# Kernel tuning notes

Hardware: AMD Instinct MI355X
Metric: run time of the kernel (lower is better)

The kernel has to match this reference:

```python
import jax, jax.numpy as jnp
import numpy as np

B = 1_000_000
S = 5          # no_sensors
I = S + 3      # linear in_features


def setup_inputs() -> dict:
    key = jax.random.key(0)
    k = jax.random.split(key, 9)
    x = jax.random.uniform(k[0], (B, S), dtype=jnp.float32)
    W1d = jax.random.normal(k[1], (B, 3, I), dtype=jnp.float32) * 0.5
    W1m = jax.random.normal(k[2], (B, 3, I), dtype=jnp.float32) * 0.5
    s1d = jax.random.uniform(k[3], (B, 3), dtype=jnp.float32)   # previous layer1d_output
    s1m = jax.random.uniform(k[4], (B, 3), dtype=jnp.float32)   # previous layer1m_output
    excitatory_rule = jnp.where(jax.random.bernoulli(k[5], 0.5, (3, I)), 1.0, -1.0).astype(jnp.float32)
    learning_rate = jnp.full((3, I), 0.05, dtype=jnp.float32)
    driving_rule = jax.random.randint(k[6], (3, I), 0, 2, dtype=jnp.int32)
    learning_rule = jax.random.randint(k[7], (3, I), 0, 4, dtype=jnp.int32)
    return {"x": x, "W1d": W1d, "W1m": W1m, "s1d": s1d, "s1m": s1m,
            "excitatory_rule": excitatory_rule, "learning_rate": learning_rate,
            "driving_rule": driving_rule, "learning_rule": learning_rule}


def reference(x, W1d, W1m, s1d, s1m, excitatory_rule, learning_rate, driving_rule, learning_rule):
    # forward (batched over B agents)
    x1 = jnp.concatenate([x, s1d], axis=1)                       # [B, I]
    x2 = jnp.concatenate([x, s1m], axis=1)                       # [B, I]
    out1 = jax.nn.sigmoid(jnp.einsum('bij,bj->bi', W1d, x1))     # driving activation
    out2 = 0.5 * jax.nn.sigmoid(jnp.einsum('bij,bj->bi', W1m, x2)) + 0.5  # modulatory

    lr = learning_rate[None]      # [1,3,I]
    rule = learning_rule[None]    # [1,3,I]
    exc = excitatory_rule[None]   # [1,3,I]

    def updated(W, xv, yv):
        # per-element Hebbian-family update, vectorized over [B,3,I]
        xb = xv[:, None, :]   # x[j] broadcast over output unit i
        yb = yv[:, :, None]   # y[i] broadcast over input j
        w = jnp.abs(W)        # torch code first assigns abs(w), then uses it in the rule
        hebb = lr * xb * yb * (1 - w)
        post = lr * (w * (xb - 1) * yb + (1 - w) * xb * yb)
        pre  = lr * (w * xb * (yb - 1) + (1 - w) * xb * yb)
        d = jnp.tanh(4 * (1 - jnp.abs(xb - yb) - 2))
        cov = lr * jnp.where(d > 0, d * (1 - w), d * w)
        delta = jnp.select([rule == 0, rule == 1, rule == 2], [hebb, post, pre], cov)
        wn = w + delta
        # sign-flip if excitatory_rule * w < 0
        return jnp.where(exc * wn < 0, wn * exc, wn)

    drive = (driving_rule == 1)[None]                            # [1,3,I]
    W1d_new = jnp.where(drive, updated(W1d, x1, out1), W1d)
    W1m_new = jnp.where(drive, W1m, updated(W1m, x2, out2))

    output = (out1 * out1)[:, 1:]                                # squared, drop unit 0 -> [B,2]
    return output, W1d_new, W1m_new, out1, out2
```

## Files before the change

kernel.cpp:

```cpp
#include <hip/hip_runtime.h>
#include <math.h>


__device__ __forceinline__ float upd_elem(float W, float xb, float yb,
                                          float lr, int rule, float exc) {
    float w = fabsf(W);
    float delta;
    if (rule == 0) {
        delta = lr * xb * yb * (1.f - w);
    } else if (rule == 1) {
        delta = lr * (w * (xb - 1.f) * yb + (1.f - w) * xb * yb);
    } else if (rule == 2) {
        delta = lr * (w * xb * (yb - 1.f) + (1.f - w) * xb * yb);
    } else {
        float d = tanhf(4.f * (1.f - fabsf(xb - yb) - 2.f));
        delta = lr * ((d > 0.f) ? d * (1.f - w) : d * w);
    }
    float wn = w + delta;
    return (exc * wn < 0.f) ? wn * exc : wn;
}

__global__ __launch_bounds__(256) void nn_plastic_kernel(
    const float* __restrict__ x,
    const float* __restrict__ W1d,
    const float* __restrict__ W1m,
    const float* __restrict__ s1d,
    const float* __restrict__ s1m,
    const float* __restrict__ exc_t,
    const float* __restrict__ lr_t,
    const int*   __restrict__ drive_t,
    const int*   __restrict__ rule_t,
    float* __restrict__ out,
    int B)
{
    int b = blockIdx.x * blockDim.x + threadIdx.x;
    if (b >= B) return;

    float x1[8], x2[8];
#pragma unroll
    for (int j = 0; j < 5; ++j) {
        float v = x[b * 5 + j];
        x1[j] = v; x2[j] = v;
    }
#pragma unroll
    for (int j = 0; j < 3; ++j) {
        x1[5 + j] = s1d[b * 3 + j];
        x2[5 + j] = s1m[b * 3 + j];
    }

    float4 wd[6], wm[6];
    const float4* W1d4 = reinterpret_cast<const float4*>(W1d) + (size_t)b * 6;
    const float4* W1m4 = reinterpret_cast<const float4*>(W1m) + (size_t)b * 6;
#pragma unroll
    for (int k = 0; k < 6; ++k) { wd[k] = W1d4[k]; wm[k] = W1m4[k]; }
    float* wdf = reinterpret_cast<float*>(wd);
    float* wmf = reinterpret_cast<float*>(wm);

    float out1[3], out2[3];
#pragma unroll
    for (int i = 0; i < 3; ++i) {
        float a1 = 0.f, a2 = 0.f;
#pragma unroll
        for (int j = 0; j < 8; ++j) {
            a1 = fmaf(wdf[i * 8 + j], x1[j], a1);
            a2 = fmaf(wmf[i * 8 + j], x2[j], a2);
        }
        out1[i] = 1.f / (1.f + expf(-a1));
        out2[i] = 0.5f / (1.f + expf(-a2)) + 0.5f;
    }

#pragma unroll
    for (int i = 0; i < 3; ++i) {
#pragma unroll
        for (int j = 0; j < 8; ++j) {
            const int k = i * 8 + j;
            const float lr  = lr_t[k];
            const float exc = exc_t[k];
            const int   rul = rule_t[k];
            const int   drv = drive_t[k];
            if (drv == 1) {
                wdf[k] = upd_elem(wdf[k], x1[j], out1[i], lr, rul, exc);
            } else {
                wmf[k] = upd_elem(wmf[k], x2[j], out2[i], lr, rul, exc);
            }
        }
    }

    float* out_o  = out;
    float* out_wd = out + (size_t)B * 2;
    float* out_wm = out + (size_t)B * 26;
    float* out_o1 = out + (size_t)B * 50;
    float* out_o2 = out + (size_t)B * 53;

    float4* wd_out4 = reinterpret_cast<float4*>(out_wd) + (size_t)b * 6;
    float4* wm_out4 = reinterpret_cast<float4*>(out_wm) + (size_t)b * 6;
#pragma unroll
    for (int k = 0; k < 6; ++k) { wd_out4[k] = wd[k]; wm_out4[k] = wm[k]; }

    float2 o = make_float2(out1[1] * out1[1], out1[2] * out1[2]);
    reinterpret_cast<float2*>(out_o)[b] = o;
#pragma unroll
    for (int i = 0; i < 3; ++i) {
        out_o1[b * 3 + i] = out1[i];
        out_o2[b * 3 + i] = out2[i];
    }
}

extern "C" void kernel_launch(void* const* d_in, const int* in_sizes, int n_in,
                              void* d_out, int out_size, void* d_ws, size_t ws_size,
                              hipStream_t stream) {
    const float* x    = (const float*)d_in[0];
    const float* W1d  = (const float*)d_in[1];
    const float* W1m  = (const float*)d_in[2];
    const float* s1d  = (const float*)d_in[3];
    const float* s1m  = (const float*)d_in[4];
    const float* exc  = (const float*)d_in[5];
    const float* lr   = (const float*)d_in[6];
    const int*   drv  = (const int*)d_in[7];
    const int*   rul  = (const int*)d_in[8];
    float* out = (float*)d_out;

    const int B = in_sizes[0] / 5;
    const int block = 256;
    const int grid = (B + block - 1) / block;
    nn_plastic_kernel<<<grid, block, 0, stream>>>(
        x, W1d, W1m, s1d, s1m, exc, lr, drv, rul, out, B);
}
```

Baseline: 410.9 us.

## Stage weight matrices through LDS with coalesced direct-to-LDS loads and stores

Each block now loads its slice of W1d and W1m into shared memory with global_load_lds in a fully coalesced pattern, and each thread reads its 24 weights from LDS. Updated weights go back to LDS and are written out coalesced after a barrier. This replaces the strided per-thread float4 accesses, which spanned 96 bytes per thread. It costs 48KB of LDS per block, adds two barriers, and the launch-bounds hint of 3 waves may limit occupancy.

Result: faster. 400.4 us (-2.6%).

```diff
diff --git a/kernel.cpp b/kernel.cpp
--- a/kernel.cpp
+++ b/kernel.cpp
@@ -1,6 +1,13 @@
 #include <hip/hip_runtime.h>
 #include <math.h>
 
+
+__device__ __forceinline__ void gload_lds16(const float* g, float* lds) {
+    __builtin_amdgcn_global_load_lds(
+        (const __attribute__((address_space(1))) void*)g,
+        (__attribute__((address_space(3))) void*)lds,
+        16, 0, 0);
+}
 
 __device__ __forceinline__ float upd_elem(float W, float xb, float yb,
                                           float lr, int rule, float exc) {
@@ -20,7 +27,7 @@
     return (exc * wn < 0.f) ? wn * exc : wn;
 }
 
-__global__ __launch_bounds__(256) void nn_plastic_kernel(
+__global__ __launch_bounds__(256, 3) void nn_plastic_kernel(
     const float* __restrict__ x,
     const float* __restrict__ W1d,
     const float* __restrict__ W1m,
@@ -33,76 +40,117 @@
     float* __restrict__ out,
     int B)
 {
-    int b = blockIdx.x * blockDim.x + threadIdx.x;
-    if (b >= B) return;
+    __shared__ float wA[6144];
+    __shared__ float wB[6144];
 
-    float x1[8], x2[8];
+    const int t = threadIdx.x;
+    const long long b      = (long long)blockIdx.x * 256 + t;
+    const long long total4 = (long long)B * 6;
+    const long long base4  = (long long)blockIdx.x * 1536;
+    const bool act = (b < (long long)B);
+
+    const float4* W1d4 = (const float4*)W1d;
+    const float4* W1m4 = (const float4*)W1m;
 #pragma unroll
-    for (int j = 0; j < 5; ++j) {
-        float v = x[b * 5 + j];
-        x1[j] = v; x2[j] = v;
-    }
-#pragma unroll
-    for (int j = 0; j < 3; ++j) {
-        x1[5 + j] = s1d[b * 3 + j];
-        x2[5 + j] = s1m[b * 3 + j];
-    }
-
-    float4 wd[6], wm[6];
-    const float4* W1d4 = reinterpret_cast<const float4*>(W1d) + (size_t)b * 6;
-    const float4* W1m4 = reinterpret_cast<const float4*>(W1m) + (size_t)b * 6;
-#pragma unroll
-    for (int k = 0; k < 6; ++k) { wd[k] = W1d4[k]; wm[k] = W1m4[k]; }
-    float* wdf = reinterpret_cast<float*>(wd);
-    float* wmf = reinterpret_cast<float*>(wm);
-
-    float out1[3], out2[3];
-#pragma unroll
-    for (int i = 0; i < 3; ++i) {
-        float a1 = 0.f, a2 = 0.f;
-#pragma unroll
-        for (int j = 0; j < 8; ++j) {
-            a1 = fmaf(wdf[i * 8 + j], x1[j], a1);
-            a2 = fmaf(wmf[i * 8 + j], x2[j], a2);
-        }
-        out1[i] = 1.f / (1.f + expf(-a1));
-        out2[i] = 0.5f / (1.f + expf(-a2)) + 0.5f;
-    }
-
-#pragma unroll
-    for (int i = 0; i < 3; ++i) {
-#pragma unroll
-        for (int j = 0; j < 8; ++j) {
-            const int k = i * 8 + j;
-            const float lr  = lr_t[k];
-            const float exc = exc_t[k];
-            const int   rul = rule_t[k];
-            const int   drv = drive_t[k];
-            if (drv == 1) {
-                wdf[k] = upd_elem(wdf[k], x1[j], out1[i], lr, rul, exc);
-            } else {
-                wmf[k] = upd_elem(wmf[k], x2[j], out2[i], lr, rul, exc);
-            }
+    for (int k = 0; k < 6; ++k) {
+        long long idx = base4 + k * 256 + t;
+        if (idx < total4) {
+            gload_lds16((const float*)(W1d4 + idx), &wA[(k * 256 + t) * 4]);
+            gload_lds16((const float*)(W1m4 + idx), &wB[(k * 256 + t) * 4]);
         }
     }
 
-    float* out_o  = out;
+    float xv[5], sdv[3], smv[3];
+    if (act) {
+#pragma unroll
+        for (int j = 0; j < 5; ++j) xv[j] = x[b * 5 + j];
+#pragma unroll
+        for (int j = 0; j < 3; ++j) { sdv[j] = s1d[b * 3 + j]; smv[j] = s1m[b * 3 + j]; }
+    }
+
+    __syncthreads();
+
+    float out1[3], out2[3];
+    if (act) {
+        float4 wd[6];
+#pragma unroll
+        for (int c = 0; c < 6; ++c) wd[c] = *(const float4*)&wA[t * 24 + c * 4];
+        float* wdf = (float*)wd;
+#pragma unroll
+        for (int i = 0; i < 3; ++i) {
+            float a = 0.f;
+#pragma unroll
+            for (int j = 0; j < 5; ++j) a = fmaf(wdf[i * 8 + j], xv[j], a);
+#pragma unroll
+            for (int j = 0; j < 3; ++j) a = fmaf(wdf[i * 8 + 5 + j], sdv[j], a);
+            out1[i] = 1.f / (1.f + expf(-a));
+        }
+#pragma unroll
+        for (int i = 0; i < 3; ++i) {
+#pragma unroll
+            for (int j = 0; j < 8; ++j) {
+                const int k = i * 8 + j;
+                if (drive_t[k] == 1) {
+                    float xb = (j < 5) ? xv[j] : sdv[j - 5];
+                    wdf[k] = upd_elem(wdf[k], xb, out1[i], lr_t[k], rule_t[k], exc_t[k]);
+                }
+            }
+        }
+#pragma unroll
+        for (int c = 0; c < 6; ++c) *(float4*)&wA[t * 24 + c * 4] = wd[c];
+
+        float4 wm[6];
+#pragma unroll
+        for (int c = 0; c < 6; ++c) wm[c] = *(const float4*)&wB[t * 24 + c * 4];
+        float* wmf = (float*)wm;
+#pragma unroll
+        for (int i = 0; i < 3; ++i) {
+            float a = 0.f;
+#pragma unroll
+            for (int j = 0; j < 5; ++j) a = fmaf(wmf[i * 8 + j], xv[j], a);
+#pragma unroll
+            for (int j = 0; j < 3; ++j) a = fmaf(wmf[i * 8 + 5 + j], smv[j], a);
+            out2[i] = 0.5f / (1.f + expf(-a)) + 0.5f;
+        }
+#pragma unroll
+        for (int i = 0; i < 3; ++i) {
+#pragma unroll
+            for (int j = 0; j < 8; ++j) {
+                const int k = i * 8 + j;
+                if (drive_t[k] != 1) {
+                    float xb = (j < 5) ? xv[j] : smv[j - 5];
+                    wmf[k] = upd_elem(wmf[k], xb, out2[i], lr_t[k], rule_t[k], exc_t[k]);
+                }
+            }
+        }
+#pragma unroll
+        for (int c = 0; c < 6; ++c) *(float4*)&wB[t * 24 + c * 4] = wm[c];
+    }
+
+    __syncthreads();
+
     float* out_wd = out + (size_t)B * 2;
     float* out_wm = out + (size_t)B * 26;
-    float* out_o1 = out + (size_t)B * 50;
-    float* out_o2 = out + (size_t)B * 53;
+    float4* out_wd4 = (float4*)out_wd;
+    float4* out_wm4 = (float4*)out_wm;
+#pragma unroll
+    for (int k = 0; k < 6; ++k) {
+        long long idx = base4 + k * 256 + t;
+        if (idx < total4) {
+            out_wd4[idx] = *(const float4*)&wA[(k * 256 + t) * 4];
+            out_wm4[idx] = *(const float4*)&wB[(k * 256 + t) * 4];
+        }
+    }
 
-    float4* wd_out4 = reinterpret_cast<float4*>(out_wd) + (size_t)b * 6;
-    float4* wm_out4 = reinterpret_cast<float4*>(out_wm) + (size_t)b * 6;
+    if (act) {
+        float* out_o1 = out + (size_t)B * 50;
+        float* out_o2 = out + (size_t)B * 53;
+        ((float2*)out)[b] = make_float2(out1[1] * out1[1], out1[2] * out1[2]);
 #pragma unroll
-    for (int k = 0; k < 6; ++k) { wd_out4[k] = wd[k]; wm_out4[k] = wm[k]; }
-
-    float2 o = make_float2(out1[1] * out1[1], out1[2] * out1[2]);
-    reinterpret_cast<float2*>(out_o)[b] = o;
-#pragma unroll
-    for (int i = 0; i < 3; ++i) {
-        out_o1[b * 3 + i] = out1[i];
-        out_o2[b * 3 + i] = out2[i];
+        for (int i = 0; i < 3; ++i) {
+            out_o1[b * 3 + i] = out1[i];
+            out_o2[b * 3 + i] = out2[i];
+        }
     }
 }
 
```
